# Optimization experiments

Measured on AMD Instinct MI355X. Metric: run time of the kernel, lower is better.

Reference implementation:

```python
import jax, jax.numpy as jnp
import numpy as np

VIEW_R = 32
SCALING = 16.0 / 8.0  # lora_alpha / r


def setup_inputs() -> dict:
    key = jax.random.key(0)
    ks = jax.random.split(key, 12)
    bs, S, d, r = 64, 256, 768, 8
    n = d // VIEW_R  # 24
    return {
        "x": jax.random.normal(ks[0], (bs, S, d), jnp.float32),
        "user_h": jax.random.normal(ks[1], (bs, d), jnp.float32),
        "item_h": jax.random.normal(ks[2], (bs, d), jnp.float32),
        "W": jax.random.normal(ks[3], (d, d), jnp.float32) * 0.02,   # base weight (out,in)
        "b": jax.random.normal(ks[4], (d,), jnp.float32) * 0.02,
        "A": jax.random.normal(ks[5], (r, d), jnp.float32) * 0.02,   # lora_A
        "B": jax.random.normal(ks[6], (d, r), jnp.float32) * 0.02,   # lora_B (zeros at init; randomized to exercise math)
        "Wu": jax.random.normal(ks[7], (d, d), jnp.float32) * 0.02,  # lora_U weight (out,in)
        "VU": jax.random.normal(ks[8], (n, VIEW_R), jnp.float32) * 0.02,
        "Wi": jax.random.normal(ks[9], (d, d), jnp.float32) * 0.02,  # lora_I weight
        "VI": jax.random.normal(ks[10], (n, VIEW_R), jnp.float32) * 0.02,
    }


def _kron_branch(x, h, Wlin, V):
    # original: weight[b, q*n_in + n, l*32 + m] = (h @ Wlin.T)[b, q, l] * V[n, m]
    #           result[b,s,:] = x[b,s,:] @ weight[b]
    # factorized form (same math, no (bs, d, d) intermediate):
    bs, S, d = x.shape
    n, m = V.shape
    q = VIEW_R
    l = d // VIEW_R
    wq = (h @ Wlin.T).reshape(bs, q, l)          # (b, q, l)
    x4 = x.reshape(bs, S, q, n)                  # d split as (q, n)
    t = jnp.einsum("bsqn,nm->bsqm", x4, V)
    out = jnp.einsum("bsqm,bql->bslm", t, wq)    # out index = l*32 + m
    return out.reshape(bs, S, d)


def reference(x, user_h, item_h, W, b, A, B, Wu, VU, Wi, VI):
    # F.linear + LoRA
    out = jnp.einsum("bsd,od->bso", x, W) + b
    out = out + jnp.einsum("bsd,rd,or->bso", x, A, B) * SCALING
    # user Kronecker low-rank per-sample weight branch
    out = out + _kron_branch(x, user_h, Wu, VU)
    # item branch
    out = out + _kron_branch(x, item_h, Wi, VI)
    return out
```

## Files before the change

### kernel.cpp

```cpp
#include <hip/hip_runtime.h>
#include <hip/hip_bf16.h>

typedef __bf16 bf16x8 __attribute__((ext_vector_type(8)));
typedef float f32x4 __attribute__((ext_vector_type(4)));
typedef unsigned short u16x8 __attribute__((ext_vector_type(8)));

__device__ __forceinline__ unsigned short f2bf(float f) {
    unsigned int u = __builtin_bit_cast(unsigned int, f);
    unsigned int r = (u + 0x7FFFu + ((u >> 16) & 1u)) >> 16;
    return (unsigned short)r;
}

__device__ __forceinline__ void load_lds_16(const void* g, void* lds) {
    __builtin_amdgcn_global_load_lds(
        (const __attribute__((address_space(1))) unsigned int*)g,
        (__attribute__((address_space(3))) unsigned int*)lds, 16, 0, 0);
}

__global__ void prep_kernel(const float* __restrict__ x, unsigned short* __restrict__ xb,
                            const float* __restrict__ W, const float* __restrict__ A,
                            const float* __restrict__ B, unsigned short* __restrict__ weffB,
                            const float* __restrict__ uh, const float* __restrict__ ih,
                            const float* __restrict__ Wu, const float* __restrict__ Wi,
                            float* __restrict__ wqu, float* __restrict__ wqi) {
    int bx = blockIdx.x;
    int t = threadIdx.x;
    if (bx < 6144) {
        int i = bx * 256 + t;
        const float4* xp = (const float4*)x;
        float4 a = xp[i * 2];
        float4 c = xp[i * 2 + 1];
        u16x8 r;
        r[0] = f2bf(a.x); r[1] = f2bf(a.y); r[2] = f2bf(a.z); r[3] = f2bf(a.w);
        r[4] = f2bf(c.x); r[5] = f2bf(c.y); r[6] = f2bf(c.z); r[7] = f2bf(c.w);
        *(u16x8*)(xb + (size_t)i * 8) = r;
    } else if (bx < 8448) {
        int idx = bx - 6144;
        int o = idx / 3;
        int k = (idx % 3) * 256 + t;
        float acc = W[o * 768 + k];
#pragma unroll
        for (int r = 0; r < 8; ++r) acc += 2.0f * B[o * 8 + r] * A[r * 768 + k];
        weffB[o * 768 + k] = f2bf(acc);
    } else {
        int b2 = bx - 8448;
        int og = b2 % 192;
        int rest = b2 / 192;
        int b = rest & 63;
        int br = rest >> 6;
        int wave = t >> 6, lane = t & 63;
        int o = og * 4 + wave;
        const float* h = (br ? ih : uh) + b * 768;
        const float* Wrow = (br ? Wi : Wu) + (size_t)o * 768;
        const float4* hp = (const float4*)(h + lane * 12);
        const float4* wp = (const float4*)(Wrow + lane * 12);
        float s = 0.0f;
#pragma unroll
        for (int j = 0; j < 3; ++j) {
            float4 hv = hp[j], wv = wp[j];
            s += hv.x * wv.x + hv.y * wv.y + hv.z * wv.z + hv.w * wv.w;
        }
#pragma unroll
        for (int off = 32; off; off >>= 1) s += __shfl_down(s, off);
        if (lane == 0) (br ? wqi : wqu)[b * 768 + o] = s;
    }
}

__global__ __launch_bounds__(256, 3) void gemm_fused_kernel(
    const unsigned short* __restrict__ Xb, const unsigned short* __restrict__ WeffB,
    const float* __restrict__ VU, const float* __restrict__ VI,
    const float* __restrict__ wqu, const float* __restrict__ wqi,
    const float* __restrict__ bias, float* __restrict__ out) {
    __shared__ __align__(16) unsigned short As[128 * 64];
    __shared__ __align__(16) unsigned short Bs[128 * 64];
    __shared__ __align__(16) unsigned short Ks[128 * 64];
    __shared__ __align__(16) unsigned int vui[32 * 26];
    __shared__ __align__(16) float wqs[32 * 8];
    __shared__ float bias_s[128];
    const int tid = threadIdx.x;
    const int wave = tid >> 6, lane = tid & 63;
    const int id = blockIdx.x;
    const int nt = id >> 7, rem = id & 127, b = rem >> 1, mt = rem & 1;
    const int s0 = mt * 128, n0 = nt * 128;

    for (int i = tid; i < 768; i += 256) {
        int n = i >> 5, m = i & 31;
        vui[m * 26 + n] = ((unsigned int)f2bf(VU[i]) << 16) | (unsigned int)f2bf(VI[i]);
    }
    {
        int q = tid >> 3, lr = (tid >> 1) & 3, br = tid & 1;
        const float* wq = br ? wqi : wqu;
        wqs[tid] = wq[b * 768 + q * 24 + nt * 4 + lr];
    }
    if (tid < 128) bias_s[tid] = bias[n0 + tid];
    __syncthreads();

    const unsigned short* Abase = Xb + (size_t)(b * 256 + s0) * 768;
    const unsigned short* Bbase = WeffB + (size_t)n0 * 768;
    const int wm = wave & 1, wn = wave >> 1;
    const int lrow = lane >> 3, lcp = lane & 7;
    const int mp = tid & 31, cp = tid >> 5;
    const int psl = cp ^ (mp & 7);

    f32x4 acc[4][4] = {};

    for (int kk = 0; kk < 768; kk += 64) {
#pragma unroll
        for (int u = 0; u < 4; ++u) {
            int tA = wave * 4 + u;
            int r = tA * 8 + lrow;
            int c = lcp ^ (r & 7);
            load_lds_16(Abase + (size_t)r * 768 + kk + c * 8, (void*)(As + tA * 512));
            load_lds_16(Bbase + (size_t)r * 768 + kk + c * 8, (void*)(Bs + tA * 512));
        }
        {
            int kb = kk + cp * 8;
            int q = (kb * 2731) >> 16;
            int n0c = kb - q * 24;
            const unsigned int* vp = &vui[mp * 26 + n0c];
            uint2 pv01 = *(const uint2*)(vp);
            uint2 pv23 = *(const uint2*)(vp + 2);
            uint2 pv45 = *(const uint2*)(vp + 4);
            uint2 pv67 = *(const uint2*)(vp + 6);
            unsigned int pv[8] = {pv01.x, pv01.y, pv23.x, pv23.y, pv45.x, pv45.y, pv67.x, pv67.y};
            float fu[8], fi[8];
#pragma unroll
            for (int j = 0; j < 8; ++j) {
                fu[j] = __builtin_bit_cast(float, pv[j] & 0xFFFF0000u);
                fi[j] = __builtin_bit_cast(float, pv[j] << 16);
            }
            const float2* wp = (const float2*)&wqs[q * 8];
#pragma unroll
            for (int lr = 0; lr < 4; ++lr) {
                float2 w = wp[lr];
                u16x8 kv;
#pragma unroll
                for (int j = 0; j < 8; ++j) {
                    float v = fu[j] * w.x + fi[j] * w.y;
                    kv[j] = (unsigned short)(__builtin_bit_cast(unsigned int, v) >> 16);
                }
                *(u16x8*)(Ks + (lr * 32 + mp) * 64 + psl * 8) = kv;
            }
        }
        __syncthreads();
#pragma unroll
        for (int h = 0; h < 2; ++h) {
            const int cb = h * 4 + (lane >> 4);
            const int rl = lane & 15;
            bf16x8 af[4], bw[4], bk[4];
#pragma unroll
            for (int i = 0; i < 4; ++i) {
                int r = wm * 64 + i * 16 + rl;
                int c = cb ^ (r & 7);
                af[i] = *(const bf16x8*)(As + r * 64 + c * 8);
            }
#pragma unroll
            for (int j = 0; j < 4; ++j) {
                int r = wn * 64 + j * 16 + rl;
                int c = cb ^ (r & 7);
                bw[j] = *(const bf16x8*)(Bs + r * 64 + c * 8);
                bk[j] = *(const bf16x8*)(Ks + r * 64 + c * 8);
            }
#pragma unroll
            for (int i = 0; i < 4; ++i)
#pragma unroll
                for (int j = 0; j < 4; ++j) {
                    acc[i][j] = __builtin_amdgcn_mfma_f32_16x16x32_bf16(af[i], bw[j], acc[i][j], 0, 0, 0);
                    acc[i][j] = __builtin_amdgcn_mfma_f32_16x16x32_bf16(af[i], bk[j], acc[i][j], 0, 0, 0);
                }
        }
        __syncthreads();
    }

    const int cl = lane & 15, rq = lane >> 4;
#pragma unroll
    for (int j = 0; j < 4; ++j) {
        int nn = wn * 64 + j * 16 + cl;
        float bv = bias_s[nn];
#pragma unroll
        for (int i = 0; i < 4; ++i) {
            int mrow = s0 + wm * 64 + i * 16 + rq * 4;
            float* op = out + (size_t)(b * 256 + mrow) * 768 + n0 + nn;
#pragma unroll
            for (int g = 0; g < 4; ++g) op[(size_t)g * 768] = acc[i][j][g] + bv;
        }
    }
}

__global__ void weff_kernel(const float* __restrict__ W, const float* __restrict__ A,
                            const float* __restrict__ B, float* __restrict__ Weff) {
    int o = blockIdx.x / 3;
    int k = (blockIdx.x % 3) * 256 + threadIdx.x;
    float acc = W[o * 768 + k];
#pragma unroll
    for (int r = 0; r < 8; ++r) acc += 2.0f * B[o * 8 + r] * A[r * 768 + k];
    Weff[o * 768 + k] = acc;
}

__global__ void wq2_kernel(const float* __restrict__ uh, const float* __restrict__ ih,
                           const float* __restrict__ Wu, const float* __restrict__ Wi,
                           float* __restrict__ wqu, float* __restrict__ wqi) {
    int bx = blockIdx.x;
    int og = bx % 192;
    int rest = bx / 192;
    int b = rest & 63;
    int br = rest >> 6;
    int wave = threadIdx.x >> 6, lane = threadIdx.x & 63;
    int o = og * 4 + wave;
    const float* h = (br ? ih : uh) + b * 768;
    const float* Wrow = (br ? Wi : Wu) + (size_t)o * 768;
    const float4* hp = (const float4*)(h + lane * 12);
    const float4* wp = (const float4*)(Wrow + lane * 12);
    float s = 0.0f;
#pragma unroll
    for (int j = 0; j < 3; ++j) {
        float4 hv = hp[j], wv = wp[j];
        s += hv.x * wv.x + hv.y * wv.y + hv.z * wv.z + hv.w * wv.w;
    }
#pragma unroll
    for (int off = 32; off; off >>= 1) s += __shfl_down(s, off);
    if (lane == 0) (br ? wqi : wqu)[b * 768 + o] = s;
}

__global__ void naive_kernel(const float* __restrict__ x, const float* __restrict__ Weff,
                             const float* __restrict__ wqu, const float* __restrict__ wqi,
                             const float* __restrict__ VU, const float* __restrict__ VI,
                             const float* __restrict__ bias, float* __restrict__ out) {
    int bs_ = blockIdx.x / 3;
    int chunk = blockIdx.x % 3;
    int b = bs_ >> 8;
    __shared__ float xs[768];
    for (int i = threadIdx.x; i < 768; i += 256) xs[i] = x[(size_t)bs_ * 768 + i];
    __syncthreads();
    int o = chunk * 256 + threadIdx.x;
    int m = o & 31, l = o >> 5;
    float acc = bias[o];
    for (int q = 0; q < 32; ++q) {
        float wu = wqu[b * 768 + q * 24 + l];
        float wi = wqi[b * 768 + q * 24 + l];
#pragma unroll
        for (int n = 0; n < 24; ++n) {
            int k = q * 24 + n;
            float w = Weff[o * 768 + k] + VU[n * 32 + m] * wu + VI[n * 32 + m] * wi;
            acc += xs[k] * w;
        }
    }
    out[(size_t)bs_ * 768 + o] = acc;
}

extern "C" void kernel_launch(void* const* d_in, const int* in_sizes, int n_in,
                              void* d_out, int out_size, void* d_ws, size_t ws_size,
                              hipStream_t stream) {
    const float* x  = (const float*)d_in[0];
    const float* uh = (const float*)d_in[1];
    const float* ih = (const float*)d_in[2];
    const float* W  = (const float*)d_in[3];
    const float* bv = (const float*)d_in[4];
    const float* A  = (const float*)d_in[5];
    const float* B  = (const float*)d_in[6];
    const float* Wu = (const float*)d_in[7];
    const float* VU = (const float*)d_in[8];
    const float* Wi = (const float*)d_in[9];
    const float* VI = (const float*)d_in[10];
    float* out = (float*)d_out;

    const size_t off_xb   = 0;
    const size_t off_weff = 25165824;
    const size_t off_wqu  = off_weff + 1179648;
    const size_t off_wqi  = off_wqu + 196608;
    const size_t need     = off_wqi + 196608;

    char* ws = (char*)d_ws;
    if (ws_size >= need) {
        unsigned short* xb    = (unsigned short*)(ws + off_xb);
        unsigned short* weffB = (unsigned short*)(ws + off_weff);
        float* wqu = (float*)(ws + off_wqu);
        float* wqi = (float*)(ws + off_wqi);
        prep_kernel<<<33024, 256, 0, stream>>>(x, xb, W, A, B, weffB, uh, ih, Wu, Wi, wqu, wqi);
        gemm_fused_kernel<<<768, 256, 0, stream>>>(xb, weffB, VU, VI, wqu, wqi, bv, out);
    } else {
        float* weff = (float*)ws;
        float* wqu  = weff + 589824;
        float* wqi  = wqu + 49152;
        weff_kernel<<<2304, 256, 0, stream>>>(W, A, B, weff);
        wq2_kernel<<<24576, 256, 0, stream>>>(uh, ih, Wu, Wi, wqu, wqi);
        naive_kernel<<<49152, 256, 0, stream>>>(x, weff, wqu, wqi, VU, VI, bv, out);
    }
}
```

Measured before the change: 177.1 us.

## Fold per-sample Kronecker weights into shared B tile, halve MFMA count

Instead of building a separate Ks tile and issuing two MFMAs per fragment pair, the kernel now loads the base effective weight into registers, adds the per-sample Kronecker term (fu*wu + fi*wi) in fp32, and writes one combined bf16 B tile into LDS. This halves MFMA work and the B-side LDS reads, and drops the Ks buffer, which could allow more waves per CU. Register prefetch of the next weight chunk replaces the async global-to-LDS load for B. The cost is more VALU work in the tile-build step, more registers, and an extra bf16 rounding of the summed weight, which slightly changes numerics.

```diff
diff --git a/kernel.cpp b/kernel.cpp
--- a/kernel.cpp
+++ b/kernel.cpp
@@ -73,7 +73,6 @@
     const float* __restrict__ bias, float* __restrict__ out) {
     __shared__ __align__(16) unsigned short As[128 * 64];
     __shared__ __align__(16) unsigned short Bs[128 * 64];
-    __shared__ __align__(16) unsigned short Ks[128 * 64];
     __shared__ __align__(16) unsigned int vui[32 * 26];
     __shared__ __align__(16) float wqs[32 * 8];
     __shared__ float bias_s[128];
@@ -88,9 +87,9 @@
         vui[m * 26 + n] = ((unsigned int)f2bf(VU[i]) << 16) | (unsigned int)f2bf(VI[i]);
     }
     {
-        int q = tid >> 3, lr = (tid >> 1) & 3, br = tid & 1;
+        int q = tid >> 3, g = (tid >> 1) & 3, br = tid & 1;
         const float* wq = br ? wqi : wqu;
-        wqs[tid] = wq[b * 768 + q * 24 + nt * 4 + lr];
+        wqs[tid] = wq[b * 768 + q * 24 + nt * 4 + g];
     }
     if (tid < 128) bias_s[tid] = bias[n0 + tid];
     __syncthreads();
@@ -99,10 +98,14 @@
     const unsigned short* Bbase = WeffB + (size_t)n0 * 768;
     const int wm = wave & 1, wn = wave >> 1;
     const int lrow = lane >> 3, lcp = lane & 7;
-    const int mp = tid & 31, cp = tid >> 5;
-    const int psl = cp ^ (mp & 7);
+    const int rg = tid >> 3, cc = tid & 7;
+    const int sl = cc ^ (rg & 7);
+    const unsigned short* Wp0 = Bbase + (size_t)rg * 768 + cc * 8;
 
     f32x4 acc[4][4] = {};
+    u16x8 wreg[4];
+#pragma unroll
+    for (int g = 0; g < 4; ++g) wreg[g] = *(const u16x8*)(Wp0 + (size_t)g * 32 * 768);
 
     for (int kk = 0; kk < 768; kk += 64) {
 #pragma unroll
@@ -111,13 +114,12 @@
             int r = tA * 8 + lrow;
             int c = lcp ^ (r & 7);
             load_lds_16(Abase + (size_t)r * 768 + kk + c * 8, (void*)(As + tA * 512));
-            load_lds_16(Bbase + (size_t)r * 768 + kk + c * 8, (void*)(Bs + tA * 512));
         }
         {
-            int kb = kk + cp * 8;
+            int kb = kk + cc * 8;
             int q = (kb * 2731) >> 16;
             int n0c = kb - q * 24;
-            const unsigned int* vp = &vui[mp * 26 + n0c];
+            const unsigned int* vp = &vui[rg * 26 + n0c];
             uint2 pv01 = *(const uint2*)(vp);
             uint2 pv23 = *(const uint2*)(vp + 2);
             uint2 pv45 = *(const uint2*)(vp + 4);
@@ -129,25 +131,34 @@
                 fu[j] = __builtin_bit_cast(float, pv[j] & 0xFFFF0000u);
                 fi[j] = __builtin_bit_cast(float, pv[j] << 16);
             }
-            const float2* wp = (const float2*)&wqs[q * 8];
-#pragma unroll
-            for (int lr = 0; lr < 4; ++lr) {
-                float2 w = wp[lr];
+            const float4* wp4 = (const float4*)&wqs[q * 8];
+            float4 wa = wp4[0], wb = wp4[1];
+            float wu[4] = {wa.x, wa.z, wb.x, wb.z};
+            float wi[4] = {wa.y, wa.w, wb.y, wb.w};
+#pragma unroll
+            for (int g = 0; g < 4; ++g) {
                 u16x8 kv;
 #pragma unroll
                 for (int j = 0; j < 8; ++j) {
-                    float v = fu[j] * w.x + fi[j] * w.y;
+                    float wf = __builtin_bit_cast(float, (unsigned int)wreg[g][j] << 16);
+                    float v = wf + fu[j] * wu[g];
+                    v = v + fi[j] * wi[g];
                     kv[j] = (unsigned short)(__builtin_bit_cast(unsigned int, v) >> 16);
                 }
-                *(u16x8*)(Ks + (lr * 32 + mp) * 64 + psl * 8) = kv;
-            }
+                *(u16x8*)(Bs + (g * 32 + rg) * 64 + sl * 8) = kv;
+            }
+        }
+        if (kk < 704) {
+            const unsigned short* Wn = Wp0 + kk + 64;
+#pragma unroll
+            for (int g = 0; g < 4; ++g) wreg[g] = *(const u16x8*)(Wn + (size_t)g * 32 * 768);
         }
         __syncthreads();
 #pragma unroll
         for (int h = 0; h < 2; ++h) {
             const int cb = h * 4 + (lane >> 4);
             const int rl = lane & 15;
-            bf16x8 af[4], bw[4], bk[4];
+            bf16x8 af[4], bw[4];
 #pragma unroll
             for (int i = 0; i < 4; ++i) {
                 int r = wm * 64 + i * 16 + rl;
@@ -159,15 +170,12 @@
                 int r = wn * 64 + j * 16 + rl;
                 int c = cb ^ (r & 7);
                 bw[j] = *(const bf16x8*)(Bs + r * 64 + c * 8);
-                bk[j] = *(const bf16x8*)(Ks + r * 64 + c * 8);
             }
 #pragma unroll
             for (int i = 0; i < 4; ++i)
 #pragma unroll
-                for (int j = 0; j < 4; ++j) {
+                for (int j = 0; j < 4; ++j)
                     acc[i][j] = __builtin_amdgcn_mfma_f32_16x16x32_bf16(af[i], bw[j], acc[i][j], 0, 0, 0);
-                    acc[i][j] = __builtin_amdgcn_mfma_f32_16x16x32_bf16(af[i], bk[j], acc[i][j], 0, 0, 0);
-                }
         }
         __syncthreads();
     }
```

Result: faster. 162.1 us (-8.5%).
